# Optimization experiments

Measured on AMD Instinct MI355X. Metric: run time of the kernel, lower is better.

## Reference

```python
import jax, jax.numpy as jnp
import numpy as np

MODEL_DIM = 1024
NUM_HEADS = 16
HEAD_DIM = MODEL_DIM // NUM_HEADS
SCALE = HEAD_DIM ** -0.5


def setup_inputs() -> dict:
    key = jax.random.key(0)
    ks = jax.random.split(key, 8)
    B, LQ, LC = 2, 2048, 2048
    # lecun-normal init: std = 1/sqrt(fan_in)
    std = MODEL_DIM ** -0.5
    return {
        "query": jax.random.normal(ks[0], (B, LQ, MODEL_DIM), jnp.float32),
        "context": jax.random.normal(ks[1], (B, LC, MODEL_DIM), jnp.float32),
        "Wq": jax.random.normal(ks[2], (MODEL_DIM, MODEL_DIM), jnp.float32) * std,
        "bq": jnp.zeros((MODEL_DIM,), jnp.float32),
        "Wkv": jax.random.normal(ks[3], (MODEL_DIM, 2 * MODEL_DIM), jnp.float32) * std,
        "bkv": jnp.zeros((2 * MODEL_DIM,), jnp.float32),
        "Wout": jax.random.normal(ks[4], (MODEL_DIM, MODEL_DIM), jnp.float32) * std,
        "bout": jnp.zeros((MODEL_DIM,), jnp.float32),
    }


def reference(query, context, Wq, bq, Wkv, bkv, Wout, bout):
    B, LQ, _ = query.shape
    LC = context.shape[1]
    H, D = NUM_HEADS, HEAD_DIM
    # projections
    q = query @ Wq + bq                      # [B, LQ, M]
    kv = context @ Wkv + bkv                 # [B, LC, 2M]
    # einops 'b s (h d c) -> c b h s d': innermost grouping order is (h, d, c)
    kv = kv.reshape(B, LC, H, D, 2)
    k = jnp.transpose(kv[..., 0], (0, 2, 1, 3))   # [B, H, LC, D]
    v = jnp.transpose(kv[..., 1], (0, 2, 1, 3))   # [B, H, LC, D]
    q = jnp.transpose(q.reshape(B, LQ, H, D), (0, 2, 1, 3))  # [B, H, LQ, D]
    # attention
    scores = jnp.einsum('bhid,bhjd->bhij', q, k) * SCALE      # [B, H, LQ, LC]
    attn = jax.nn.softmax(scores, axis=-1)
    out = jnp.einsum('bhij,bhjd->bhid', attn, v)              # [B, H, LQ, D]
    out = jnp.transpose(out, (0, 2, 1, 3)).reshape(B, LQ, H * D)
    return out @ Wout + bout
```

## Files before the change

kernel.cpp:

```cpp
#include <hip/hip_runtime.h>
#include <hip/hip_bf16.h>
#include <stdint.h>

typedef __bf16 bf16_t;
typedef __bf16 bf16x8 __attribute__((ext_vector_type(8)));
typedef __bf16 bf16x4_t __attribute__((ext_vector_type(4)));
typedef float f32x4 __attribute__((ext_vector_type(4)));
typedef float f32x16 __attribute__((ext_vector_type(16)));
typedef unsigned int u32x4 __attribute__((ext_vector_type(4)));

#define B_   2
#define H_   16
#define D_   64
#define LQ_  2048
#define LC_  2048
#define M_   1024

#define EXP2(x) __builtin_amdgcn_exp2f(x)


__device__ __forceinline__ void gload_lds16(const void* g, void* l) {
  __builtin_amdgcn_global_load_lds((__attribute__((address_space(1))) unsigned int*)(g),
                                   (__attribute__((address_space(3))) unsigned int*)(l),
                                   16, 0, 0);
}

__device__ __forceinline__ unsigned pack2(float a, float b) {
  __bf16 x = (__bf16)a, y = (__bf16)b;
  unsigned short ux = __builtin_bit_cast(unsigned short, x);
  unsigned short uy = __builtin_bit_cast(unsigned short, y);
  return (unsigned)ux | ((unsigned)uy << 16);
}

__global__ void prep_kernel(const float* __restrict__ query, const float* __restrict__ context,
                            bf16_t* __restrict__ queryb, bf16_t* __restrict__ ctxb,
                            const float* __restrict__ Wq, const float* __restrict__ Wkv,
                            const float* __restrict__ Wout,
                            bf16_t* __restrict__ Wq_t, bf16_t* __restrict__ Wkv_t,
                            bf16_t* __restrict__ Wout_t) {
  __shared__ float tile[32][33];
  const int bid = blockIdx.x;
  if (bid < 8192) {
    const int n4each = 4096 * 1024 / 4;
    int i = bid * 256 + threadIdx.x;
    const float* in = (i < n4each) ? query : context;
    bf16_t* out = (i < n4each) ? queryb : ctxb;
    const int j = (i < n4each) ? i : (i - n4each);
    const float4 f = ((const float4*)in)[j];
    bf16x4_t o4;
    o4[0] = (__bf16)f.x; o4[1] = (__bf16)f.y; o4[2] = (__bf16)f.z; o4[3] = (__bf16)f.w;
    ((bf16x4_t*)out)[j] = o4;
    return;
  }
  int tb = bid - 8192;
  const float* in; bf16_t* out; int N, kvperm;
  if (tb < 1024)      { in = Wq;   out = Wq_t;   N = 1024; kvperm = 0; }
  else if (tb < 3072) { tb -= 1024; in = Wkv;  out = Wkv_t;  N = 2048; kvperm = 1; }
  else                { tb -= 3072; in = Wout; out = Wout_t; N = 1024; kvperm = 0; }
  const int K = 1024;
  const int nb = N / 32;
  const int n0 = (tb % nb) * 32, k0 = (tb / nb) * 32;
  const int tx = threadIdx.x & 31, ty = threadIdx.x >> 5;
  #pragma unroll
  for (int r = ty; r < 32; r += 8)
    tile[r][tx] = in[(size_t)(k0 + r) * N + (n0 + tx)];
  __syncthreads();
  #pragma unroll
  for (int r = ty; r < 32; r += 8) {
    const int n = n0 + r;
    const int orow = kvperm ? ((n & ~127) | ((n & 1) << 6) | ((n >> 1) & 63)) : n;
    out[(size_t)orow * K + (k0 + tx)] = (__bf16)tile[tx][r];
  }
}

__global__ __launch_bounds__(256, 3)
void proj_fused_kernel(const bf16_t* __restrict__ Aq, const bf16_t* __restrict__ Akv,
                       const bf16_t* __restrict__ Wq_t, const bf16_t* __restrict__ Wkv_t,
                       const float* __restrict__ bq, const float* __restrict__ bkv,
                       bf16_t* __restrict__ q_s, bf16_t* __restrict__ k_s,
                       bf16_t* __restrict__ v_t) {
  __shared__ __attribute__((aligned(16))) bf16_t ldsA[2][128 * 64];
  __shared__ __attribute__((aligned(16))) bf16_t ldsB[2][64 * 64];
  const int tid  = threadIdx.x;
  const int wave = tid >> 6, lane = tid & 63;
  const int bid  = blockIdx.x + 48 * blockIdx.y;
  const int nbid = (bid & 7) * 192 + (bid >> 3);
  const int ny = nbid / 48, nx = nbid % 48;
  const bool isq = (nx < 16);
  const bf16_t* A  = isq ? Aq : Akv;
  const bf16_t* Bt = isq ? Wq_t : Wkv_t;
  const int n0 = (isq ? nx : (nx - 16)) * 64;
  const int m0 = ny * 128;
  const int K  = 1024;
  const int wr = wave >> 1, wc = wave & 1;
  const int lrow = lane & 15, lg = lane >> 4;
  const int srow = lane >> 3;
  const int sc8  = ((lane & 7) ^ srow) * 8;

#define PSTAGE(T, BUF) do {                                                      \
    const int kk_ = (T) * 64;                                                    \
    _Pragma("unroll")                                                            \
    for (int i_ = 0; i_ < 4; ++i_) {                                             \
      const int c_ = wave * 4 + i_;                                              \
      gload_lds16(A + (size_t)(m0 + c_ * 8 + srow) * K + (kk_ + sc8),            \
                  ldsA[BUF] + c_ * 512);                                         \
    }                                                                            \
    _Pragma("unroll")                                                            \
    for (int i_ = 0; i_ < 2; ++i_) {                                             \
      const int c_ = wave * 2 + i_;                                              \
      gload_lds16(Bt + (size_t)(n0 + c_ * 8 + srow) * K + (kk_ + sc8),           \
                  ldsB[BUF] + c_ * 512);                                         \
    }                                                                            \
  } while (0)

  f32x4 acc[4][2] = {};

  PSTAGE(0, 0);
  asm volatile("s_waitcnt vmcnt(0)" ::: "memory");
  __builtin_amdgcn_s_barrier();
  PSTAGE(1, 1);

  #pragma unroll 1
  for (int kt = 0; kt < 16; ++kt) {
    const int buf = kt & 1;
    bf16x8 af[2][4], bfv[2][2];
    #pragma unroll
    for (int ks = 0; ks < 2; ++ks) {
      #pragma unroll
      for (int mi = 0; mi < 4; ++mi)
        af[ks][mi] = *(const bf16x8*)(ldsA[buf] + (wr * 64 + mi * 16 + lrow) * 64 +
                                      (((ks * 4 + lg) ^ (lrow & 7)) * 8));
      #pragma unroll
      for (int ni = 0; ni < 2; ++ni)
        bfv[ks][ni] = *(const bf16x8*)(ldsB[buf] + (wc * 32 + ni * 16 + lrow) * 64 +
                                       (((ks * 4 + lg) ^ (lrow & 7)) * 8));
    }
    asm volatile("s_waitcnt lgkmcnt(0)" ::: "memory");
    __builtin_amdgcn_sched_barrier(0);
    __builtin_amdgcn_s_barrier();

    int t2 = kt + 2; if (t2 > 15) t2 = 15;
    PSTAGE(t2, buf);

    #pragma unroll
    for (int ks = 0; ks < 2; ++ks)
      #pragma unroll
      for (int mi = 0; mi < 4; ++mi)
        #pragma unroll
        for (int ni = 0; ni < 2; ++ni)
          acc[mi][ni] = __builtin_amdgcn_mfma_f32_16x16x32_bf16(af[ks][mi], bfv[ks][ni],
                                                                acc[mi][ni], 0, 0, 0);

    asm volatile("s_waitcnt vmcnt(6)" ::: "memory");
    __builtin_amdgcn_sched_barrier(0);
    __builtin_amdgcn_s_barrier();
  }
#undef PSTAGE

  #pragma unroll
  for (int mi = 0; mi < 4; ++mi) {
    const int rbase = m0 + wr * 64 + mi * 16 + lg * 4;
    #pragma unroll
    for (int ni = 0; ni < 2; ++ni) {
      const int col = n0 + wc * 32 + ni * 16 + lrow;
      if (isq) {
        const float bv = bq[col];
        #pragma unroll
        for (int j = 0; j < 4; ++j)
          q_s[(size_t)(rbase + j) * 1024 + col] =
              (__bf16)((acc[mi][ni][j] + bv) * 0.18033688011112042f);
      } else {
        const int hh = col >> 7, cbit = (col >> 6) & 1, d = col & 63;
        const float bv = bkv[hh * 128 + d * 2 + cbit];
        #pragma unroll
        for (int j = 0; j < 4; ++j) {
          const int row = rbase + j;
          const int bi = row >> 11, lc = row & 2047;
          const float val = acc[mi][ni][j] + bv;
          if (cbit == 0)
            k_s[((size_t)(bi * 16 + hh) * 2048 + lc) * 64 + d] = (__bf16)val;
          else
            v_t[(((size_t)(bi * 16 + hh) * 64 + (lc >> 5)) * 64 + d) * 32 + (lc & 31)] = (__bf16)val;
        }
      }
    }
  }
}

__global__ __launch_bounds__(256, 3)
void gemm_out_kernel(const bf16_t* __restrict__ A, const bf16_t* __restrict__ Bt,
                     const float* __restrict__ bias, float* __restrict__ out0) {
  __shared__ __attribute__((aligned(16))) bf16_t ldsA[2][128 * 64];
  __shared__ __attribute__((aligned(16))) bf16_t ldsB[2][64 * 64];
  const int tid  = threadIdx.x;
  const int wave = tid >> 6, lane = tid & 63;
  const int bid  = blockIdx.x + 16 * blockIdx.y;
  const int nbid = (bid & 7) * 64 + (bid >> 3);
  const int m0 = (nbid >> 4) * 128, n0 = (nbid & 15) * 64;
  const int K = 1024, N = 1024;
  const int wr = wave >> 1, wc = wave & 1;
  const int lrow = lane & 15, lg = lane >> 4;
  const int srow = lane >> 3;
  const int sc8  = ((lane & 7) ^ srow) * 8;

#define OSTAGE(T, BUF) do {                                                      \
    const int kk_ = (T) * 64;                                                    \
    _Pragma("unroll")                                                            \
    for (int i_ = 0; i_ < 4; ++i_) {                                             \
      const int c_ = wave * 4 + i_;                                              \
      gload_lds16(A + (size_t)(m0 + c_ * 8 + srow) * K + (kk_ + sc8),            \
                  ldsA[BUF] + c_ * 512);                                         \
    }                                                                            \
    _Pragma("unroll")                                                            \
    for (int i_ = 0; i_ < 2; ++i_) {                                             \
      const int c_ = wave * 2 + i_;                                              \
      gload_lds16(Bt + (size_t)(n0 + c_ * 8 + srow) * K + (kk_ + sc8),           \
                  ldsB[BUF] + c_ * 512);                                         \
    }                                                                            \
  } while (0)

  f32x4 acc[4][2] = {};

  OSTAGE(0, 0);
  asm volatile("s_waitcnt vmcnt(0)" ::: "memory");
  __builtin_amdgcn_s_barrier();
  OSTAGE(1, 1);

  #pragma unroll 1
  for (int kt = 0; kt < 16; ++kt) {
    const int buf = kt & 1;
    bf16x8 af[2][4], bfv[2][2];
    #pragma unroll
    for (int ks = 0; ks < 2; ++ks) {
      #pragma unroll
      for (int mi = 0; mi < 4; ++mi)
        af[ks][mi] = *(const bf16x8*)(ldsA[buf] + (wr * 64 + mi * 16 + lrow) * 64 +
                                      (((ks * 4 + lg) ^ (lrow & 7)) * 8));
      #pragma unroll
      for (int ni = 0; ni < 2; ++ni)
        bfv[ks][ni] = *(const bf16x8*)(ldsB[buf] + (wc * 32 + ni * 16 + lrow) * 64 +
                                       (((ks * 4 + lg) ^ (lrow & 7)) * 8));
    }
    asm volatile("s_waitcnt lgkmcnt(0)" ::: "memory");
    __builtin_amdgcn_sched_barrier(0);
    __builtin_amdgcn_s_barrier();

    int t2 = kt + 2; if (t2 > 15) t2 = 15;
    OSTAGE(t2, buf);

    #pragma unroll
    for (int ks = 0; ks < 2; ++ks)
      #pragma unroll
      for (int mi = 0; mi < 4; ++mi)
        #pragma unroll
        for (int ni = 0; ni < 2; ++ni)
          acc[mi][ni] = __builtin_amdgcn_mfma_f32_16x16x32_bf16(af[ks][mi], bfv[ks][ni],
                                                                acc[mi][ni], 0, 0, 0);

    asm volatile("s_waitcnt vmcnt(6)" ::: "memory");
    __builtin_amdgcn_sched_barrier(0);
    __builtin_amdgcn_s_barrier();
  }
#undef OSTAGE

  #pragma unroll
  for (int mi = 0; mi < 4; ++mi) {
    const int rbase = m0 + wr * 64 + mi * 16 + lg * 4;
    #pragma unroll
    for (int ni = 0; ni < 2; ++ni) {
      const int col = n0 + wc * 32 + ni * 16 + lrow;
      const float bv = bias[col];
      #pragma unroll
      for (int j = 0; j < 4; ++j)
        out0[(size_t)(rbase + j) * N + col] = acc[mi][ni][j] + bv;
    }
  }
}

__global__ __launch_bounds__(256, 2)
void attn_kernel(const bf16_t* __restrict__ q, const bf16_t* __restrict__ k,
                 const bf16_t* __restrict__ vt, bf16_t* __restrict__ o) {
  __shared__ __attribute__((aligned(16))) bf16_t stage[4][2048];
  __shared__ float Osh[64][64];
  __shared__ float Lsh[4][2][32];

  const int tid  = threadIdx.x;
  const int wave = tid >> 6, lane = tid & 63;
  const int li = lane & 31, hi = lane >> 5;

  const int bid  = blockIdx.x;
  const int xcd  = bid & 7, slot = bid >> 3;
  const int bh   = xcd * 4 + (slot >> 5);
  const int qt   = slot & 31;
  const int b    = bh >> 4, h = bh & 15;

  bf16x8 qa[2][4];
  #pragma unroll
  for (int g = 0; g < 2; ++g) {
    const bf16_t* qp = q + (size_t)(b * LQ_ + qt * 64 + g * 32 + li) * 1024 + h * 64 + hi * 8;
    #pragma unroll
    for (int ks = 0; ks < 4; ++ks) qa[g][ks] = *(const bf16x8*)(qp + ks * 16);
  }
  asm volatile("s_waitcnt vmcnt(0)" ::: "memory");

  const int kv0 = wave * (LC_ / 4);
  const bf16_t* kbase  = k  + (size_t)bh * LC_ * 64 + (size_t)kv0 * 64;
  const bf16_t* vtbase = vt + ((size_t)bh * 64 + wave * 16) * 2048;

  const size_t koff = (size_t)(lane >> 3) * 64 + (size_t)(((lane & 7) ^ (lane >> 3)) * 8);

  bf16_t* lk = &stage[wave][0];

#define STAGE_K(T) do {                                                          \
    const bf16_t* kc_ = kbase + (size_t)(T) * 2048;                              \
    _Pragma("unroll")                                                            \
    for (int i_ = 0; i_ < 4; ++i_)                                               \
      gload_lds16(kc_ + koff + (size_t)i_ * 512, lk + i_ * 512);                 \
  } while (0)

  f32x16 oaccA[2] = {};
  f32x16 oaccB[2] = {};
  float l_run0 = 0.f, l_run1 = 0.f;

  STAGE_K(0);

  #pragma unroll 1
  for (int t = 0; t < 16; ++t) {
    asm volatile("s_waitcnt vmcnt(0)" ::: "memory");
    __builtin_amdgcn_sched_barrier(0);

    bf16x8 vf[2][2];
    {
      const bf16_t* vtile = vtbase + (size_t)t * 2048;
      #pragma unroll
      for (int dt = 0; dt < 2; ++dt)
        #pragma unroll
        for (int ks2 = 0; ks2 < 2; ++ks2)
          vf[dt][ks2] = *(const bf16x8*)(vtile + (dt * 32 + li) * 32 + ks2 * 16 + hi * 8);
    }
    __builtin_amdgcn_sched_barrier(0);

    bf16x8 kf[4];
    #pragma unroll
    for (int ks = 0; ks < 4; ++ks)
      kf[ks] = *(const bf16x8*)(lk + li * 64 + (((hi + ks * 2) ^ (li & 7)) * 8));

    asm volatile("s_waitcnt lgkmcnt(0)" ::: "memory");
    __builtin_amdgcn_sched_barrier(0);

    int t2 = t + 1; if (t2 > 15) t2 = 15;
    STAGE_K(t2);

    #pragma unroll
    for (int g = 0; g < 2; ++g) {
      f32x16 sacc = {};
      __builtin_amdgcn_s_setprio(1);
      #pragma unroll
      for (int ks = 0; ks < 4; ++ks)
        sacc = __builtin_amdgcn_mfma_f32_32x32x16_bf16(kf[ks], qa[g][ks], sacc, 0, 0, 0);
      __builtin_amdgcn_s_setprio(0);

      float pv[16]; float ps = 0.f;
      #pragma unroll
      for (int r = 0; r < 16; ++r) { pv[r] = EXP2(sacc[r]); ps += pv[r]; }
      ps += __shfl_xor(ps, 32, 64);
      if (g == 0) l_run0 += ps; else l_run1 += ps;

      unsigned pk[8];
      #pragma unroll
      for (int i = 0; i < 8; ++i) pk[i] = pack2(pv[2 * i], pv[2 * i + 1]);

      unsigned w[8];
      #pragma unroll
      for (int g2 = 0; g2 < 2; ++g2) {
        const int bx = g2 * 4;
        #pragma unroll
        for (int ii = 0; ii < 2; ++ii) {
          const unsigned lo = pk[bx + ii], hi2 = pk[bx + 2 + ii];
          const unsigned s  = hi ? lo : hi2;
          const unsigned xs = __shfl_xor(s, 32, 64);
          w[bx + ii]     = hi ? xs  : lo;
          w[bx + 2 + ii] = hi ? hi2 : xs;
        }
      }
      const u32x4 pw0 = {w[0], w[1], w[2], w[3]};
      const u32x4 pw1 = {w[4], w[5], w[6], w[7]};
      const bf16x8 pb0 = __builtin_bit_cast(bf16x8, pw0);
      const bf16x8 pb1 = __builtin_bit_cast(bf16x8, pw1);

      __builtin_amdgcn_s_setprio(1);
      if (g == 0) {
        #pragma unroll
        for (int dt = 0; dt < 2; ++dt) {
          oaccA[dt] = __builtin_amdgcn_mfma_f32_32x32x16_bf16(vf[dt][0], pb0, oaccA[dt], 0, 0, 0);
          oaccA[dt] = __builtin_amdgcn_mfma_f32_32x32x16_bf16(vf[dt][1], pb1, oaccA[dt], 0, 0, 0);
        }
      } else {
        #pragma unroll
        for (int dt = 0; dt < 2; ++dt) {
          oaccB[dt] = __builtin_amdgcn_mfma_f32_32x32x16_bf16(vf[dt][0], pb0, oaccB[dt], 0, 0, 0);
          oaccB[dt] = __builtin_amdgcn_mfma_f32_32x32x16_bf16(vf[dt][1], pb1, oaccB[dt], 0, 0, 0);
        }
      }
      __builtin_amdgcn_s_setprio(0);
    }
  }
#undef STAGE_K

  if (hi == 0) { Lsh[wave][0][li] = l_run0; Lsh[wave][1][li] = l_run1; }
  __syncthreads();

  #pragma unroll
  for (int ss = 0; ss < 4; ++ss) {
    if (wave == ss) {
      #pragma unroll
      for (int g = 0; g < 2; ++g)
        #pragma unroll
        for (int dt = 0; dt < 2; ++dt)
          #pragma unroll
          for (int r = 0; r < 16; ++r) {
            const int d = dt * 32 + (r & 3) + 8 * (r >> 2) + 4 * hi;
            const float val = (g == 0) ? oaccA[dt][r] : oaccB[dt][r];
            if (ss == 0) Osh[d][g * 32 + li] = val;
            else         Osh[d][g * 32 + li] += val;
          }
    }
    __syncthreads();
  }

  #pragma unroll
  for (int rr = 0; rr < 2; ++rr) {
    const int qq = tid >> 3, c8 = (tid & 7) * 8;
    const float lg = Lsh[0][rr][qq] + Lsh[1][rr][qq] + Lsh[2][rr][qq] + Lsh[3][rr][qq];
    const float rl = 1.f / lg;
    u32x4 ow;
    #pragma unroll
    for (int j = 0; j < 4; ++j)
      ow[j] = pack2(Osh[c8 + 2 * j][rr * 32 + qq] * rl, Osh[c8 + 2 * j + 1][rr * 32 + qq] * rl);
    *(u32x4*)(o + (size_t)(b * LQ_ + qt * 64 + rr * 32 + qq) * 1024 + h * 64 + c8) = ow;
  }
}

extern "C" void kernel_launch(void* const* d_in, const int* in_sizes, int n_in,
                              void* d_out, int out_size, void* d_ws, size_t ws_size,
                              hipStream_t stream) {
  const float* query   = (const float*)d_in[0];
  const float* context = (const float*)d_in[1];
  const float* Wq      = (const float*)d_in[2];
  const float* bq      = (const float*)d_in[3];
  const float* Wkv     = (const float*)d_in[4];
  const float* bkv     = (const float*)d_in[5];
  const float* Wout    = (const float*)d_in[6];
  const float* bout    = (const float*)d_in[7];

  char* p = (char*)d_ws;
  bf16_t* queryb = (bf16_t*)p; p += (size_t)4096 * 1024 * 2;
  bf16_t* ctxb   = (bf16_t*)p; p += (size_t)4096 * 1024 * 2;
  bf16_t* Wq_t   = (bf16_t*)p; p += (size_t)1024 * 1024 * 2;
  bf16_t* Wkv_t  = (bf16_t*)p; p += (size_t)2048 * 1024 * 2;
  bf16_t* Wout_t = (bf16_t*)p; p += (size_t)1024 * 1024 * 2;
  bf16_t* q_s    = (bf16_t*)p; p += (size_t)4096 * 1024 * 2;
  bf16_t* k_s    = (bf16_t*)p; p += (size_t)4096 * 1024 * 2;
  bf16_t* v_t    = (bf16_t*)p; p += (size_t)4096 * 1024 * 2;
  bf16_t* attnb  = (bf16_t*)p; p += (size_t)4096 * 1024 * 2;
  if ((size_t)(p - (char*)d_ws) > ws_size) return;

  prep_kernel<<<12288, 256, 0, stream>>>(query, context, queryb, ctxb,
                                         Wq, Wkv, Wout, Wq_t, Wkv_t, Wout_t);
  proj_fused_kernel<<<dim3(48, 32), 256, 0, stream>>>(queryb, ctxb, Wq_t, Wkv_t,
                                                      bq, bkv, q_s, k_s, v_t);
  attn_kernel<<<dim3(1024), 256, 0, stream>>>(q_s, k_s, v_t, attnb);
  gemm_out_kernel<<<dim3(16, 32), 256, 0, stream>>>(attnb, Wout_t, bout, (float*)d_out);
}
```

Before: 144.4 us.

## Permute K rows at load time to eliminate P cross-lane shuffles

Stages K tiles into LDS with a permuted row order, so the S accumulator rows come out already in the layout the PV MFMA needs. This removes the per-tile shuffle exchange that reorganised packed probabilities across the two half-waves. The row-sum reduction across halves is also hoisted out of the loop to a single shuffle at the end. Correctness depends on the permutation matching the MFMA output layout exactly.

```diff
diff --git a/kernel.cpp b/kernel.cpp
--- a/kernel.cpp
+++ b/kernel.cpp
@@ -307,7 +307,15 @@
   const bf16_t* kbase  = k  + (size_t)bh * LC_ * 64 + (size_t)kv0 * 64;
   const bf16_t* vtbase = vt + ((size_t)bh * 64 + wave * 16) * 2048;
 
-  const size_t koff = (size_t)(lane >> 3) * 64 + (size_t)(((lane & 7) ^ (lane >> 3)) * 8);
+  const int srow8 = lane >> 3;
+  const int scol  = ((lane & 7) ^ srow8) * 8;
+  size_t koffp[4];
+  #pragma unroll
+  for (int i = 0; i < 4; ++i) {
+    const int p  = i * 8 + srow8;
+    const int Lp = (((p >> 2) ^ (p >> 3)) & 1) ? (p ^ 12) : p;
+    koffp[i] = (size_t)Lp * 64 + scol;
+  }
 
   bf16_t* lk = &stage[wave][0];
 
@@ -315,7 +323,7 @@
     const bf16_t* kc_ = kbase + (size_t)(T) * 2048;                              \
     _Pragma("unroll")                                                            \
     for (int i_ = 0; i_ < 4; ++i_)                                               \
-      gload_lds16(kc_ + koff + (size_t)i_ * 512, lk + i_ * 512);                 \
+      gload_lds16(kc_ + koffp[i_], lk + i_ * 512);                               \
   } while (0)
 
   f32x16 oaccA[2] = {};
@@ -363,28 +371,12 @@
       float pv[16]; float ps = 0.f;
       #pragma unroll
       for (int r = 0; r < 16; ++r) { pv[r] = EXP2(sacc[r]); ps += pv[r]; }
-      ps += __shfl_xor(ps, 32, 64);
       if (g == 0) l_run0 += ps; else l_run1 += ps;
 
-      unsigned pk[8];
-      #pragma unroll
-      for (int i = 0; i < 8; ++i) pk[i] = pack2(pv[2 * i], pv[2 * i + 1]);
-
-      unsigned w[8];
-      #pragma unroll
-      for (int g2 = 0; g2 < 2; ++g2) {
-        const int bx = g2 * 4;
-        #pragma unroll
-        for (int ii = 0; ii < 2; ++ii) {
-          const unsigned lo = pk[bx + ii], hi2 = pk[bx + 2 + ii];
-          const unsigned s  = hi ? lo : hi2;
-          const unsigned xs = __shfl_xor(s, 32, 64);
-          w[bx + ii]     = hi ? xs  : lo;
-          w[bx + 2 + ii] = hi ? hi2 : xs;
-        }
-      }
-      const u32x4 pw0 = {w[0], w[1], w[2], w[3]};
-      const u32x4 pw1 = {w[4], w[5], w[6], w[7]};
+      const u32x4 pw0 = {pack2(pv[0], pv[1]),  pack2(pv[2], pv[3]),
+                         pack2(pv[4], pv[5]),  pack2(pv[6], pv[7])};
+      const u32x4 pw1 = {pack2(pv[8], pv[9]),  pack2(pv[10], pv[11]),
+                         pack2(pv[12], pv[13]), pack2(pv[14], pv[15])};
       const bf16x8 pb0 = __builtin_bit_cast(bf16x8, pw0);
       const bf16x8 pb1 = __builtin_bit_cast(bf16x8, pw1);
 
@@ -406,6 +398,9 @@
     }
   }
 #undef STAGE_K
+
+  l_run0 += __shfl_xor(l_run0, 32, 64);
+  l_run1 += __shfl_xor(l_run1, 32, 64);
 
   if (hi == 0) { Lsh[wave][0][li] = l_run0; Lsh[wave][1][li] = l_run1; }
   __syncthreads();
```

Measured after the change: 139.0 us. 3.7% less time.
